# Kernel optimization log

Measured on AMD Instinct MI355X. Metric: run time of the kernel, lower is better.

## Reference

```python
import jax, jax.numpy as jnp
import numpy as np

N = 50000
E = 800000
EPS = 1e-16
NEG_SLOPE = 0.2

def setup_inputs() -> dict:
    key = jax.random.key(0)
    ks = jax.random.split(key, 10)
    s = lambda fan: 1.0 / np.sqrt(fan)
    return {
        "x": jax.random.normal(ks[0], (N, 128), dtype=jnp.float32),
        "edge_index": jax.random.randint(ks[1], (2, E), 0, N, dtype=jnp.int64),
        "W1": jax.random.normal(ks[2], (128, 4 * 32), dtype=jnp.float32) * s(128),
        "att_src1": jax.random.normal(ks[3], (4, 32), dtype=jnp.float32) * s(32),
        "att_dst1": jax.random.normal(ks[4], (4, 32), dtype=jnp.float32) * s(32),
        "b1": jnp.zeros((128,), dtype=jnp.float32),
        "W2": jax.random.normal(ks[5], (128, 2), dtype=jnp.float32) * s(128),
        "att_src2": jax.random.normal(ks[6], (1, 2), dtype=jnp.float32) * s(2),
        "att_dst2": jax.random.normal(ks[7], (1, 2), dtype=jnp.float32) * s(2),
        "b2": jnp.zeros((2,), dtype=jnp.float32),
    }

def _gat_conv(x, src, dst, W, att_src, att_dst, bias, heads, out_ch, concat):
    n = x.shape[0]
    h = (x @ W).reshape(n, heads, out_ch)                      # [N,H,C]
    a_src = jnp.sum(h * att_src[None], axis=-1)                # [N,H]
    a_dst = jnp.sum(h * att_dst[None], axis=-1)                # [N,H]
    e = jax.nn.leaky_relu(a_src[src] + a_dst[dst], NEG_SLOPE)  # [Etot,H]
    # segment softmax over incoming edges per destination node
    m = jax.ops.segment_max(e, dst, num_segments=n)            # [N,H]
    m = jnp.where(jnp.isfinite(m), m, 0.0)
    ex = jnp.exp(e - m[dst])
    denom = jax.ops.segment_sum(ex, dst, num_segments=n)       # [N,H]
    alpha = ex / (denom[dst] + EPS)                            # [Etot,H]
    out = jax.ops.segment_sum(alpha[:, :, None] * h[src], dst, num_segments=n)  # [N,H,C]
    if concat:
        out = out.reshape(n, heads * out_ch)
    else:
        out = out.mean(axis=1)
    return out + bias

def reference(x, edge_index, W1, att_src1, att_dst1, b1, W2, att_src2, att_dst2, b2):
    n = x.shape[0]
    # PyG GATConv adds self-loops by default
    loops = jnp.arange(n, dtype=edge_index.dtype)
    src = jnp.concatenate([edge_index[0], loops])
    dst = jnp.concatenate([edge_index[1], loops])
    # dropout is identity at inference
    h = jax.nn.elu(_gat_conv(x, src, dst, W1, att_src1, att_dst1, b1, 4, 32, True))
    h = _gat_conv(h, src, dst, W2, att_src2, att_dst2, b2, 1, 2, False)
    return jax.nn.log_softmax(h, axis=1)
```

## Files before the change

### kernel.cpp

```cpp
#include <hip/hip_runtime.h>
#include <hip/hip_bf16.h>

#define NN 50000
#define EE 800000
#define ET (EE + NN)
#define CAP 64
#define NEG_SLOPE 0.2f
#define EPSF 1e-16f

typedef unsigned int uint32;
typedef __attribute__((ext_vector_type(8))) short short8;
typedef __attribute__((ext_vector_type(4))) float floatx4;

__device__ __forceinline__ unsigned short f2bf(float f) {
  unsigned int u = __float_as_uint(f);
  unsigned int r = (u + 0x7fffu + ((u >> 16) & 1u)) >> 16;
  return (unsigned short)r;
}
__device__ __forceinline__ float bf_lo(uint32 v) { return __uint_as_float(v << 16); }
__device__ __forceinline__ float bf_hi(uint32 v) { return __uint_as_float(v & 0xffff0000u); }

__global__ __launch_bounds__(256) void build_k(const int* __restrict__ ei,
                                               int* __restrict__ counts,
                                               int* __restrict__ csr,
                                               const float* __restrict__ W1,
                                               unsigned short* __restrict__ Wt) {
  int g = blockIdx.x * 256 + threadIdx.x;
  if (g < 128 * 128) {
    int k = g >> 7, c = g & 127;
    Wt[c * 128 + k] = f2bf(W1[g]);
  }

  const int range = blockIdx.x & 7;
  const int lo = range * (NN / 8);
  const int hi = lo + (NN / 8);
  const int group = blockIdx.x >> 3;
  const int ngr = gridDim.x >> 3;
  for (int i = group * 256 + threadIdx.x; i < ET; i += ngr * 256) {
    int d = (i < EE) ? ei[EE + i] : (i - EE);
    if (d >= lo && d < hi) {
      int s = (i < EE) ? ei[i] : d;
      int r = atomicAdd(&counts[d], 1);
      if (r < CAP) csr[d * CAP + r] = s;
    }
  }
}

__global__ __launch_bounds__(256) void gemm1_k(
    const float* __restrict__ x, const unsigned short* __restrict__ Wt,
    const float* __restrict__ att_src1, const float* __restrict__ att_dst1,
    uint32* __restrict__ h1b, float* __restrict__ as1, float* __restrict__ ad1) {
  const int t    = threadIdx.x;
  const int wave = t >> 6;
  const int lane = t & 63;
  const int quad = lane >> 4;
  const int col  = lane & 15;
  const int nodeBase = blockIdx.x * 64 + wave * 16;

  floatx4 acc[8];
  #pragma unroll
  for (int i = 0; i < 8; i++) acc[i] = (floatx4){0.f, 0.f, 0.f, 0.f};

  int mread = nodeBase + col; if (mread >= NN) mread = NN - 1;
  const float* __restrict__ xrow = x + (size_t)mread * 128 + quad * 8;
  const unsigned short* __restrict__ bbase = Wt + col * 128 + quad * 8;

  #pragma unroll
  for (int ks = 0; ks < 4; ks++) {
    float4 a0 = *(const float4*)(xrow + ks * 32);
    float4 a1 = *(const float4*)(xrow + ks * 32 + 4);
    union { short8 v; unsigned short u[8]; } af;
    af.u[0] = f2bf(a0.x); af.u[1] = f2bf(a0.y);
    af.u[2] = f2bf(a0.z); af.u[3] = f2bf(a0.w);
    af.u[4] = f2bf(a1.x); af.u[5] = f2bf(a1.y);
    af.u[6] = f2bf(a1.z); af.u[7] = f2bf(a1.w);
    #pragma unroll
    for (int tt = 0; tt < 8; tt++) {
      short8 bf = *(const short8*)(bbase + tt * 16 * 128 + ks * 32);
      acc[tt] = __builtin_amdgcn_mfma_f32_16x16x32_bf16(af.v, bf, acc[tt], 0, 0, 0);
    }
  }

  float asv[8], adv[8];
  #pragma unroll
  for (int tt = 0; tt < 8; tt++) {
    asv[tt] = att_src1[tt * 16 + col];
    adv[tt] = att_dst1[tt * 16 + col];
  }

  #pragma unroll
  for (int r = 0; r < 4; r++) {
    const int gn = nodeBase + quad * 4 + r;
    const bool live = (gn < NN);
    #pragma unroll
    for (int tt = 0; tt < 8; tt++) {
      float v = acc[tt][r];
      float w = __shfl_xor(v, 1, 64);
      if (live && ((col & 1) == 0)) {
        uint32 pk = (uint32)f2bf(v) | ((uint32)f2bf(w) << 16);
        h1b[(size_t)gn * 64 + tt * 8 + (col >> 1)] = pk;
      }
    }
    #pragma unroll
    for (int h = 0; h < 4; h++) {
      float ps = acc[2 * h][r] * asv[2 * h] + acc[2 * h + 1][r] * asv[2 * h + 1];
      float pd = acc[2 * h][r] * adv[2 * h] + acc[2 * h + 1][r] * adv[2 * h + 1];
      #pragma unroll
      for (int off = 1; off < 16; off <<= 1) {
        ps += __shfl_xor(ps, off, 64);
        pd += __shfl_xor(pd, off, 64);
      }
      if (live && col == 0) {
        as1[gn * 4 + h] = ps;
        ad1[gn * 4 + h] = pd;
      }
    }
  }
}

__global__ __launch_bounds__(256) void agg1_k(
    const int* __restrict__ counts, const int* __restrict__ csr,
    const uint32* __restrict__ h1b, const float* __restrict__ as1,
    const float* __restrict__ ad1, const float* __restrict__ b1,
    const float* __restrict__ W2, const float* __restrict__ att_src2,
    const float* __restrict__ att_dst2,
    float* __restrict__ h2, float* __restrict__ as2, float* __restrict__ ad2) {
  const int lane = threadIdx.x & 63;
  const int n = __builtin_amdgcn_readfirstlane(blockIdx.x * 4 + (threadIdx.x >> 6));
  const int hd = lane >> 4;

  const int cnt = __builtin_amdgcn_readfirstlane(counts[n]);
  const int* __restrict__ row = csr + n * CAP;
  const float adv = ad1[n * 4 + hd];

  float den = 0.f, accx = 0.f, accy = 0.f;
  int j = 0;
  for (; j + 3 < cnt; j += 4) {
    int s0 = row[j], s1 = row[j + 1], s2 = row[j + 2], s3 = row[j + 3];
    float e0 = as1[s0 * 4 + hd] + adv;
    float e1 = as1[s1 * 4 + hd] + adv;
    float e2 = as1[s2 * 4 + hd] + adv;
    float e3 = as1[s3 * 4 + hd] + adv;
    uint32 v0 = h1b[s0 * 64 + lane];
    uint32 v1 = h1b[s1 * 64 + lane];
    uint32 v2 = h1b[s2 * 64 + lane];
    uint32 v3 = h1b[s3 * 64 + lane];
    e0 = (e0 > 0.f) ? e0 : NEG_SLOPE * e0;
    e1 = (e1 > 0.f) ? e1 : NEG_SLOPE * e1;
    e2 = (e2 > 0.f) ? e2 : NEG_SLOPE * e2;
    e3 = (e3 > 0.f) ? e3 : NEG_SLOPE * e3;
    float x0 = __expf(e0), x1 = __expf(e1), x2 = __expf(e2), x3 = __expf(e3);
    den += (x0 + x1) + (x2 + x3);
    accx = fmaf(x0, bf_lo(v0), accx);
    accy = fmaf(x0, bf_hi(v0), accy);
    accx = fmaf(x1, bf_lo(v1), accx);
    accy = fmaf(x1, bf_hi(v1), accy);
    accx = fmaf(x2, bf_lo(v2), accx);
    accy = fmaf(x2, bf_hi(v2), accy);
    accx = fmaf(x3, bf_lo(v3), accx);
    accy = fmaf(x3, bf_hi(v3), accy);
  }
  for (; j < cnt; j++) {
    int s = row[j];
    float e = as1[s * 4 + hd] + adv;
    e = (e > 0.f) ? e : NEG_SLOPE * e;
    float ex = __expf(e);
    uint32 v = h1b[s * 64 + lane];
    den += ex;
    accx = fmaf(ex, bf_lo(v), accx);
    accy = fmaf(ex, bf_hi(v), accy);
  }

  float inv = 1.f / (den + EPSF);
  float2 bb = ((const float2*)b1)[lane];
  float ox = accx * inv + bb.x;
  float oy = accy * inv + bb.y;
  ox = (ox > 0.f) ? ox : (__expf(ox) - 1.f);
  oy = (oy > 0.f) ? oy : (__expf(oy) - 1.f);

  float4 wq = ((const float4*)W2)[lane];
  float p0 = ox * wq.x + oy * wq.z;
  float p1 = ox * wq.y + oy * wq.w;
  #pragma unroll
  for (int off = 32; off; off >>= 1) {
    p0 += __shfl_xor(p0, off, 64);
    p1 += __shfl_xor(p1, off, 64);
  }
  if (lane == 0) {
    *(float2*)&h2[n * 2] = make_float2(p0, p1);
    as2[n] = p0 * att_src2[0] + p1 * att_src2[1];
    ad2[n] = p0 * att_dst2[0] + p1 * att_dst2[1];
  }
}

__global__ __launch_bounds__(256) void agg2_k(
    const int* __restrict__ counts, const int* __restrict__ csr,
    const float* __restrict__ h2, const float* __restrict__ as2,
    const float* __restrict__ ad2, const float* __restrict__ b2,
    float* __restrict__ out) {
  int t = blockIdx.x * 256 + threadIdx.x;
  int n = t >> 3;
  int sub = t & 7;
  if (n >= NN) return;
  const float adv = ad2[n];
  const int cnt = counts[n];
  const int* __restrict__ row = csr + n * CAP;
  const float2* __restrict__ h2v = (const float2*)h2;

  float den = 0.f, a0 = 0.f, a1 = 0.f;
  for (int j = sub; j < cnt; j += 8) {
    int s = row[j];
    float e = as2[s] + adv;
    e = (e > 0.f) ? e : NEG_SLOPE * e;
    float ex = __expf(e);
    float2 hv = h2v[s];
    den += ex;
    a0 = fmaf(ex, hv.x, a0);
    a1 = fmaf(ex, hv.y, a1);
  }
  #pragma unroll
  for (int off = 4; off; off >>= 1) {
    den += __shfl_down(den, off, 8);
    a0  += __shfl_down(a0, off, 8);
    a1  += __shfl_down(a1, off, 8);
  }
  if (sub == 0) {
    float inv = 1.f / (den + EPSF);
    float o0 = a0 * inv + b2[0];
    float o1 = a1 * inv + b2[1];
    float mx = fmaxf(o0, o1);
    float lse = mx + __logf(__expf(o0 - mx) + __expf(o1 - mx));
    *(float2*)&out[n * 2] = make_float2(o0 - lse, o1 - lse);
  }
}

extern "C" void kernel_launch(void* const* d_in, const int* in_sizes, int n_in,
                              void* d_out, int out_size, void* d_ws, size_t ws_size,
                              hipStream_t stream) {
  const float* x        = (const float*)d_in[0];
  const int*   ei       = (const int*)d_in[1];
  const float* W1       = (const float*)d_in[2];
  const float* att_src1 = (const float*)d_in[3];
  const float* att_dst1 = (const float*)d_in[4];
  const float* b1       = (const float*)d_in[5];
  const float* W2       = (const float*)d_in[6];
  const float* att_src2 = (const float*)d_in[7];
  const float* att_dst2 = (const float*)d_in[8];
  const float* b2       = (const float*)d_in[9];
  float* out = (float*)d_out;

  char* p = (char*)d_ws;
  auto alloc = [&](size_t bytes) {
    char* r = p;
    p += (bytes + 255) & ~size_t(255);
    return r;
  };
  uint32* h1b  = (uint32*)alloc(sizeof(uint32) * NN * 64);
  float* as1   = (float*)alloc(sizeof(float) * NN * 4);
  float* ad1   = (float*)alloc(sizeof(float) * NN * 4);
  float* h2    = (float*)alloc(sizeof(float) * NN * 2);
  float* as2   = (float*)alloc(sizeof(float) * NN);
  float* ad2   = (float*)alloc(sizeof(float) * NN);
  int*   counts = (int*)alloc(sizeof(int) * NN);
  int*   csr   = (int*)alloc(sizeof(int) * NN * CAP);
  unsigned short* Wt = (unsigned short*)alloc(sizeof(unsigned short) * 128 * 128);

  hipMemsetAsync(counts, 0, sizeof(int) * NN, stream);

  build_k<<<4096, 256, 0, stream>>>(ei, counts, csr, W1, Wt);
  gemm1_k<<<(NN + 63) / 64, 256, 0, stream>>>(x, Wt, att_src1, att_dst1, h1b, as1, ad1);
  agg1_k<<<(NN + 3) / 4, 256, 0, stream>>>(counts, csr, h1b, as1, ad1, b1, W2,
                                           att_src2, att_dst2, h2, as2, ad2);
  agg2_k<<<(NN * 8 + 255) / 256, 256, 0, stream>>>(counts, csr, h2, as2, ad2, b2, out);
}
```

Measured before the change: 197.0 us.

## Fuse all GAT stages into one cooperative persistent kernel with grid syncs

Replaces the memset plus four separate kernel launches with a single cooperative persistent kernel. The stages run in grid-stride loops separated by grid.sync(), and the CSR build is overlapped with the GEMM inside the same phase. The aim is to remove launch overhead and the inter-kernel gaps. In exchange it adds grid-wide barriers, caps occupancy through launch_bounds(256,4) and a block count of at most 2048, and adds host-side property and occupancy queries on every call. A fallback multi-kernel path runs if the cooperative launch fails.

```diff
diff --git a/kernel.cpp b/kernel.cpp
--- a/kernel.cpp
+++ b/kernel.cpp
@@ -1,5 +1,8 @@
 #include <hip/hip_runtime.h>
 #include <hip/hip_bf16.h>
+#include <hip/hip_cooperative_groups.h>
+
+namespace cg = cooperative_groups;
 
 #define NN 50000
 #define EE 800000
@@ -20,22 +23,15 @@
 __device__ __forceinline__ float bf_lo(uint32 v) { return __uint_as_float(v << 16); }
 __device__ __forceinline__ float bf_hi(uint32 v) { return __uint_as_float(v & 0xffff0000u); }
 
-__global__ __launch_bounds__(256) void build_k(const int* __restrict__ ei,
-                                               int* __restrict__ counts,
-                                               int* __restrict__ csr,
-                                               const float* __restrict__ W1,
-                                               unsigned short* __restrict__ Wt) {
-  int g = blockIdx.x * 256 + threadIdx.x;
-  if (g < 128 * 128) {
-    int k = g >> 7, c = g & 127;
-    Wt[c * 128 + k] = f2bf(W1[g]);
-  }
-
-  const int range = blockIdx.x & 7;
+
+__device__ __forceinline__ void do_build(int b, int nb, const int* __restrict__ ei,
+                                         int* __restrict__ counts,
+                                         int* __restrict__ csr) {
+  const int range = b & 7;
   const int lo = range * (NN / 8);
   const int hi = lo + (NN / 8);
-  const int group = blockIdx.x >> 3;
-  const int ngr = gridDim.x >> 3;
+  const int group = b >> 3;
+  const int ngr = nb >> 3;
   for (int i = group * 256 + threadIdx.x; i < ET; i += ngr * 256) {
     int d = (i < EE) ? ei[EE + i] : (i - EE);
     if (d >= lo && d < hi) {
@@ -46,8 +42,8 @@
   }
 }
 
-__global__ __launch_bounds__(256) void gemm1_k(
-    const float* __restrict__ x, const unsigned short* __restrict__ Wt,
+__device__ __forceinline__ void do_gemm_tile(
+    int tile, const float* __restrict__ x, const unsigned short* __restrict__ Wt,
     const float* __restrict__ att_src1, const float* __restrict__ att_dst1,
     uint32* __restrict__ h1b, float* __restrict__ as1, float* __restrict__ ad1) {
   const int t    = threadIdx.x;
@@ -55,7 +51,7 @@
   const int lane = t & 63;
   const int quad = lane >> 4;
   const int col  = lane & 15;
-  const int nodeBase = blockIdx.x * 64 + wave * 16;
+  const int nodeBase = tile * 64 + wave * 16;
 
   floatx4 acc[8];
   #pragma unroll
@@ -118,16 +114,17 @@
   }
 }
 
-__global__ __launch_bounds__(256) void agg1_k(
-    const int* __restrict__ counts, const int* __restrict__ csr,
+__device__ __forceinline__ void do_agg1_group(
+    int g, const int* __restrict__ counts, const int* __restrict__ csr,
     const uint32* __restrict__ h1b, const float* __restrict__ as1,
     const float* __restrict__ ad1, const float* __restrict__ b1,
     const float* __restrict__ W2, const float* __restrict__ att_src2,
     const float* __restrict__ att_dst2,
     float* __restrict__ h2, float* __restrict__ as2, float* __restrict__ ad2) {
   const int lane = threadIdx.x & 63;
-  const int n = __builtin_amdgcn_readfirstlane(blockIdx.x * 4 + (threadIdx.x >> 6));
+  const int wv = threadIdx.x >> 6;
   const int hd = lane >> 4;
+  const int n = __builtin_amdgcn_readfirstlane(g * 4 + wv);
 
   const int cnt = __builtin_amdgcn_readfirstlane(counts[n]);
   const int* __restrict__ row = csr + n * CAP;
@@ -193,15 +190,13 @@
   }
 }
 
-__global__ __launch_bounds__(256) void agg2_k(
-    const int* __restrict__ counts, const int* __restrict__ csr,
+__device__ __forceinline__ void do_agg2_item(
+    int i, const int* __restrict__ counts, const int* __restrict__ csr,
     const float* __restrict__ h2, const float* __restrict__ as2,
     const float* __restrict__ ad2, const float* __restrict__ b2,
     float* __restrict__ out) {
-  int t = blockIdx.x * 256 + threadIdx.x;
-  int n = t >> 3;
-  int sub = t & 7;
-  if (n >= NN) return;
+  int n = i >> 3;
+  int sub = i & 7;
   const float adv = ad2[n];
   const int cnt = counts[n];
   const int* __restrict__ row = csr + n * CAP;
@@ -232,6 +227,81 @@
     float lse = mx + __logf(__expf(o0 - mx) + __expf(o1 - mx));
     *(float2*)&out[n * 2] = make_float2(o0 - lse, o1 - lse);
   }
+}
+
+__global__ __launch_bounds__(256, 4) void fused_k(
+    const float* __restrict__ x, const int* __restrict__ ei,
+    const float* __restrict__ W1, const float* __restrict__ att_src1,
+    const float* __restrict__ att_dst1, const float* __restrict__ b1,
+    const float* __restrict__ W2, const float* __restrict__ att_src2,
+    const float* __restrict__ att_dst2, const float* __restrict__ b2,
+    float* __restrict__ out,
+    uint32* __restrict__ h1b, float* __restrict__ as1, float* __restrict__ ad1,
+    float* __restrict__ h2, float* __restrict__ as2, float* __restrict__ ad2,
+    int* __restrict__ counts, int* __restrict__ csr,
+    unsigned short* __restrict__ Wt) {
+  cg::grid_group grid = cg::this_grid();
+  const int t = threadIdx.x;
+  const int b = blockIdx.x;
+  const int nb = gridDim.x;
+
+  for (int i = b * 256 + t; i < NN; i += nb * 256) counts[i] = 0;
+  for (int i = b * 256 + t; i < 128 * 128; i += nb * 256) {
+    int k = i >> 7, c = i & 127;
+    Wt[c * 128 + k] = f2bf(W1[i]);
+  }
+  grid.sync();
+
+  do_build(b, nb, ei, counts, csr);
+  for (int tile = b; tile * 64 < NN; tile += nb)
+    do_gemm_tile(tile, x, Wt, att_src1, att_dst1, h1b, as1, ad1);
+  grid.sync();
+
+  for (int g = b; g < NN / 4; g += nb)
+    do_agg1_group(g, counts, csr, h1b, as1, ad1, b1, W2, att_src2, att_dst2,
+                  h2, as2, ad2);
+  grid.sync();
+
+  for (int i = b * 256 + t; i < NN * 8; i += nb * 256)
+    do_agg2_item(i, counts, csr, h2, as2, ad2, b2, out);
+}
+
+__global__ __launch_bounds__(256) void fb_build_k(
+    const int* __restrict__ ei, int* __restrict__ counts, int* __restrict__ csr,
+    const float* __restrict__ W1, unsigned short* __restrict__ Wt) {
+  int g = blockIdx.x * 256 + threadIdx.x;
+  if (g < 128 * 128) {
+    int k = g >> 7, c = g & 127;
+    Wt[c * 128 + k] = f2bf(W1[g]);
+  }
+  do_build(blockIdx.x, gridDim.x, ei, counts, csr);
+}
+
+__global__ __launch_bounds__(256) void fb_gemm_k(
+    const float* __restrict__ x, const unsigned short* __restrict__ Wt,
+    const float* __restrict__ att_src1, const float* __restrict__ att_dst1,
+    uint32* __restrict__ h1b, float* __restrict__ as1, float* __restrict__ ad1) {
+  do_gemm_tile(blockIdx.x, x, Wt, att_src1, att_dst1, h1b, as1, ad1);
+}
+
+__global__ __launch_bounds__(256) void fb_agg1_k(
+    const int* __restrict__ counts, const int* __restrict__ csr,
+    const uint32* __restrict__ h1b, const float* __restrict__ as1,
+    const float* __restrict__ ad1, const float* __restrict__ b1,
+    const float* __restrict__ W2, const float* __restrict__ att_src2,
+    const float* __restrict__ att_dst2,
+    float* __restrict__ h2, float* __restrict__ as2, float* __restrict__ ad2) {
+  do_agg1_group(blockIdx.x, counts, csr, h1b, as1, ad1, b1, W2,
+                att_src2, att_dst2, h2, as2, ad2);
+}
+
+__global__ __launch_bounds__(256) void fb_agg2_k(
+    const int* __restrict__ counts, const int* __restrict__ csr,
+    const float* __restrict__ h2, const float* __restrict__ as2,
+    const float* __restrict__ ad2, const float* __restrict__ b2,
+    float* __restrict__ out) {
+  int i = blockIdx.x * 256 + threadIdx.x;
+  if (i < NN * 8) do_agg2_item(i, counts, csr, h2, as2, ad2, b2, out);
 }
 
 extern "C" void kernel_launch(void* const* d_in, const int* in_sizes, int n_in,
@@ -265,11 +335,41 @@
   int*   csr   = (int*)alloc(sizeof(int) * NN * CAP);
   unsigned short* Wt = (unsigned short*)alloc(sizeof(unsigned short) * 128 * 128);
 
-  hipMemsetAsync(counts, 0, sizeof(int) * NN, stream);
-
-  build_k<<<4096, 256, 0, stream>>>(ei, counts, csr, W1, Wt);
-  gemm1_k<<<(NN + 63) / 64, 256, 0, stream>>>(x, Wt, att_src1, att_dst1, h1b, as1, ad1);
-  agg1_k<<<(NN + 3) / 4, 256, 0, stream>>>(counts, csr, h1b, as1, ad1, b1, W2,
-                                           att_src2, att_dst2, h2, as2, ad2);
-  agg2_k<<<(NN * 8 + 255) / 256, 256, 0, stream>>>(counts, csr, h2, as2, ad2, b2, out);
-}
+  int dev = 0;
+  (void)hipGetDevice(&dev);
+  hipDeviceProp_t prop;
+  hipError_t pe = hipGetDeviceProperties(&prop, dev);
+  int maxBlocksPerCU = 0;
+  hipError_t oe = hipOccupancyMaxActiveBlocksPerMultiprocessor(
+      &maxBlocksPerCU, fused_k, 256, 0);
+
+  hipError_t le = hipErrorUnknown;
+  if (pe == hipSuccess && oe == hipSuccess && maxBlocksPerCU > 0) {
+    int nb = maxBlocksPerCU * prop.multiProcessorCount;
+    if (nb > 2048) nb = 2048;
+    nb &= ~7;
+    if (nb >= 8) {
+      void* args[] = {
+        (void*)&x, (void*)&ei, (void*)&W1, (void*)&att_src1, (void*)&att_dst1,
+        (void*)&b1, (void*)&W2, (void*)&att_src2, (void*)&att_dst2, (void*)&b2,
+        (void*)&out,
+        (void*)&h1b, (void*)&as1, (void*)&ad1, (void*)&h2, (void*)&as2,
+        (void*)&ad2, (void*)&counts, (void*)&csr, (void*)&Wt,
+      };
+      le = hipLaunchCooperativeKernel((const void*)fused_k, dim3(nb), dim3(256),
+                                      args, 0, stream);
+    }
+  }
+
+  if (le != hipSuccess) {
+    (void)hipGetLastError();
+    hipMemsetAsync(counts, 0, sizeof(int) * NN, stream);
+    fb_build_k<<<4096, 256, 0, stream>>>(ei, counts, csr, W1, Wt);
+    fb_gemm_k<<<(NN + 63) / 64, 256, 0, stream>>>(x, Wt, att_src1, att_dst1,
+                                                  h1b, as1, ad1);
+    fb_agg1_k<<<NN / 4, 256, 0, stream>>>(counts, csr, h1b, as1, ad1, b1, W2,
+                                          att_src2, att_dst2, h2, as2, ad2);
+    fb_agg2_k<<<(NN * 8 + 255) / 256, 256, 0, stream>>>(counts, csr, h2, as2,
+                                                        ad2, b2, out);
+  }
+}
```

New measurement: 477.5 us. 2.42x slower.

## Fuse CSR build and GEMM into one launch, replace memset with prep kernel

Applied to the files above, without the earlier changes.

The memset and the W1 transpose move into a small prep kernel. The CSR build and the first-layer GEMM now run as independent block ranges of a single launch, so the two can overlap on the device and one launch boundary disappears. This trades a kernel boundary for mixed block roles. The GEMM blocks are scheduled after 4096 build blocks, so their start may be delayed.

```diff
diff --git a/kernel.cpp b/kernel.cpp
--- a/kernel.cpp
+++ b/kernel.cpp
@@ -7,6 +7,8 @@
 #define CAP 64
 #define NEG_SLOPE 0.2f
 #define EPSF 1e-16f
+#define BUILD_BLOCKS 4096
+#define GEMM_BLOCKS ((NN + 63) / 64)
 
 typedef unsigned int uint32;
 typedef __attribute__((ext_vector_type(8))) short short8;
@@ -20,22 +22,15 @@
 __device__ __forceinline__ float bf_lo(uint32 v) { return __uint_as_float(v << 16); }
 __device__ __forceinline__ float bf_hi(uint32 v) { return __uint_as_float(v & 0xffff0000u); }
 
-__global__ __launch_bounds__(256) void build_k(const int* __restrict__ ei,
-                                               int* __restrict__ counts,
-                                               int* __restrict__ csr,
-                                               const float* __restrict__ W1,
-                                               unsigned short* __restrict__ Wt) {
-  int g = blockIdx.x * 256 + threadIdx.x;
-  if (g < 128 * 128) {
-    int k = g >> 7, c = g & 127;
-    Wt[c * 128 + k] = f2bf(W1[g]);
-  }
-
-  const int range = blockIdx.x & 7;
+
+__device__ __forceinline__ void do_build(int b, int nb, const int* __restrict__ ei,
+                                         int* __restrict__ counts,
+                                         int* __restrict__ csr) {
+  const int range = b & 7;
   const int lo = range * (NN / 8);
   const int hi = lo + (NN / 8);
-  const int group = blockIdx.x >> 3;
-  const int ngr = gridDim.x >> 3;
+  const int group = b >> 3;
+  const int ngr = nb >> 3;
   for (int i = group * 256 + threadIdx.x; i < ET; i += ngr * 256) {
     int d = (i < EE) ? ei[EE + i] : (i - EE);
     if (d >= lo && d < hi) {
@@ -46,8 +41,8 @@
   }
 }
 
-__global__ __launch_bounds__(256) void gemm1_k(
-    const float* __restrict__ x, const unsigned short* __restrict__ Wt,
+__device__ __forceinline__ void do_gemm_tile(
+    int tile, const float* __restrict__ x, const unsigned short* __restrict__ Wt,
     const float* __restrict__ att_src1, const float* __restrict__ att_dst1,
     uint32* __restrict__ h1b, float* __restrict__ as1, float* __restrict__ ad1) {
   const int t    = threadIdx.x;
@@ -55,7 +50,7 @@
   const int lane = t & 63;
   const int quad = lane >> 4;
   const int col  = lane & 15;
-  const int nodeBase = blockIdx.x * 64 + wave * 16;
+  const int nodeBase = tile * 64 + wave * 16;
 
   floatx4 acc[8];
   #pragma unroll
@@ -118,16 +113,17 @@
   }
 }
 
-__global__ __launch_bounds__(256) void agg1_k(
-    const int* __restrict__ counts, const int* __restrict__ csr,
+__device__ __forceinline__ void do_agg1_group(
+    int g, const int* __restrict__ counts, const int* __restrict__ csr,
     const uint32* __restrict__ h1b, const float* __restrict__ as1,
     const float* __restrict__ ad1, const float* __restrict__ b1,
     const float* __restrict__ W2, const float* __restrict__ att_src2,
     const float* __restrict__ att_dst2,
     float* __restrict__ h2, float* __restrict__ as2, float* __restrict__ ad2) {
   const int lane = threadIdx.x & 63;
-  const int n = __builtin_amdgcn_readfirstlane(blockIdx.x * 4 + (threadIdx.x >> 6));
+  const int wv = threadIdx.x >> 6;
   const int hd = lane >> 4;
+  const int n = __builtin_amdgcn_readfirstlane(g * 4 + wv);
 
   const int cnt = __builtin_amdgcn_readfirstlane(counts[n]);
   const int* __restrict__ row = csr + n * CAP;
@@ -193,15 +189,13 @@
   }
 }
 
-__global__ __launch_bounds__(256) void agg2_k(
-    const int* __restrict__ counts, const int* __restrict__ csr,
+__device__ __forceinline__ void do_agg2_item(
+    int i, const int* __restrict__ counts, const int* __restrict__ csr,
     const float* __restrict__ h2, const float* __restrict__ as2,
     const float* __restrict__ ad2, const float* __restrict__ b2,
     float* __restrict__ out) {
-  int t = blockIdx.x * 256 + threadIdx.x;
-  int n = t >> 3;
-  int sub = t & 7;
-  if (n >= NN) return;
+  int n = i >> 3;
+  int sub = i & 7;
   const float adv = ad2[n];
   const int cnt = counts[n];
   const int* __restrict__ row = csr + n * CAP;
@@ -232,6 +226,50 @@
     float lse = mx + __logf(__expf(o0 - mx) + __expf(o1 - mx));
     *(float2*)&out[n * 2] = make_float2(o0 - lse, o1 - lse);
   }
+}
+
+__global__ __launch_bounds__(256) void prep_zero_k(
+    const float* __restrict__ W1, unsigned short* __restrict__ Wt,
+    int* __restrict__ counts) {
+  const int step = gridDim.x * 256;
+  for (int i = blockIdx.x * 256 + threadIdx.x; i < NN; i += step) counts[i] = 0;
+  for (int i = blockIdx.x * 256 + threadIdx.x; i < 128 * 128; i += step) {
+    int k = i >> 7, c = i & 127;
+    Wt[c * 128 + k] = f2bf(W1[i]);
+  }
+}
+
+__global__ __launch_bounds__(256) void work_k(
+    const int* __restrict__ ei, int* __restrict__ counts, int* __restrict__ csr,
+    const float* __restrict__ x, const unsigned short* __restrict__ Wt,
+    const float* __restrict__ att_src1, const float* __restrict__ att_dst1,
+    uint32* __restrict__ h1b, float* __restrict__ as1, float* __restrict__ ad1) {
+  const int b = blockIdx.x;
+  if (b < BUILD_BLOCKS) {
+    do_build(b, BUILD_BLOCKS, ei, counts, csr);
+  } else {
+    do_gemm_tile(b - BUILD_BLOCKS, x, Wt, att_src1, att_dst1, h1b, as1, ad1);
+  }
+}
+
+__global__ __launch_bounds__(256) void agg1_k(
+    const int* __restrict__ counts, const int* __restrict__ csr,
+    const uint32* __restrict__ h1b, const float* __restrict__ as1,
+    const float* __restrict__ ad1, const float* __restrict__ b1,
+    const float* __restrict__ W2, const float* __restrict__ att_src2,
+    const float* __restrict__ att_dst2,
+    float* __restrict__ h2, float* __restrict__ as2, float* __restrict__ ad2) {
+  do_agg1_group(blockIdx.x, counts, csr, h1b, as1, ad1, b1, W2,
+                att_src2, att_dst2, h2, as2, ad2);
+}
+
+__global__ __launch_bounds__(256) void agg2_k(
+    const int* __restrict__ counts, const int* __restrict__ csr,
+    const float* __restrict__ h2, const float* __restrict__ as2,
+    const float* __restrict__ ad2, const float* __restrict__ b2,
+    float* __restrict__ out) {
+  int i = blockIdx.x * 256 + threadIdx.x;
+  if (i < NN * 8) do_agg2_item(i, counts, csr, h2, as2, ad2, b2, out);
 }
 
 extern "C" void kernel_launch(void* const* d_in, const int* in_sizes, int n_in,
@@ -265,11 +303,11 @@
   int*   csr   = (int*)alloc(sizeof(int) * NN * CAP);
   unsigned short* Wt = (unsigned short*)alloc(sizeof(unsigned short) * 128 * 128);
 
-  hipMemsetAsync(counts, 0, sizeof(int) * NN, stream);
-
-  build_k<<<4096, 256, 0, stream>>>(ei, counts, csr, W1, Wt);
-  gemm1_k<<<(NN + 63) / 64, 256, 0, stream>>>(x, Wt, att_src1, att_dst1, h1b, as1, ad1);
-  agg1_k<<<(NN + 3) / 4, 256, 0, stream>>>(counts, csr, h1b, as1, ad1, b1, W2,
-                                           att_src2, att_dst2, h2, as2, ad2);
-  agg2_k<<<(NN * 8 + 255) / 256, 256, 0, stream>>>(counts, csr, h2, as2, ad2, b2, out);
-}
+  prep_zero_k<<<256, 256, 0, stream>>>(W1, Wt, counts);
+  work_k<<<BUILD_BLOCKS + GEMM_BLOCKS, 256, 0, stream>>>(
+      ei, counts, csr, x, Wt, att_src1, att_dst1, h1b, as1, ad1);
+  agg1_k<<<NN / 4, 256, 0, stream>>>(counts, csr, h1b, as1, ad1, b1, W2,
+                                     att_src2, att_dst2, h2, as2, ad2);
+  agg2_k<<<(NN * 8 + 255) / 256, 256, 0, stream>>>(counts, csr, h2, as2, ad2,
+                                                   b2, out);
+}
```

Result: no change. 195.8 us (-0.6%).
